# Kernel tuning notes

Measured on AMD Instinct MI355X. Metric: run time of the kernel, lower is better.

The kernel has to match this reference:

```python
import jax, jax.numpy as jnp
import numpy as np

N = 50000
E = 800000
DIM = 256
H = 8
D = DIM // H


def setup_inputs() -> dict:
    key = jax.random.key(0)
    ks = jax.random.split(key, 12)
    s = 1.0 / np.sqrt(DIM)
    return {
        "x": jax.random.normal(ks[0], (N, DIM), dtype=jnp.float32),
        "Wq": jax.random.normal(ks[1], (DIM, DIM), dtype=jnp.float32) * s,
        "bq": jax.random.normal(ks[2], (DIM,), dtype=jnp.float32) * 0.01,
        "Wk": jax.random.normal(ks[3], (DIM, DIM), dtype=jnp.float32) * s,
        "bk": jax.random.normal(ks[4], (DIM,), dtype=jnp.float32) * 0.01,
        "Wv": jax.random.normal(ks[5], (DIM, DIM), dtype=jnp.float32) * s,
        "bv": jax.random.normal(ks[6], (DIM,), dtype=jnp.float32) * 0.01,
        "Wo": jax.random.normal(ks[7], (DIM, DIM), dtype=jnp.float32) * s,
        "bo": jax.random.normal(ks[8], (DIM,), dtype=jnp.float32) * 0.01,
        "src": jax.random.randint(ks[9], (E,), 0, N, dtype=jnp.int32),
        "dst": jax.random.randint(ks[10], (E,), 0, N, dtype=jnp.int32),
    }


def reference(x, Wq, bq, Wk, bk, Wv, bv, Wo, bo, src, dst):
    # Linear projections (torch Linear: x @ W.T + b), then [N, H, D]
    q = (x @ Wq.T + bq).reshape(N, H, D)
    k = (x @ Wk.T + bk).reshape(N, H, D)
    v = (x @ Wv.T + bv).reshape(N, H, D)

    # u_dot_v: per-edge dot(queries[src], keys[dst]) -> [E, H]
    scores = jnp.einsum('ehd,ehd->eh', q[src], k[dst]) / jnp.sqrt(jnp.float32(D))

    # edge_softmax over incoming edges of each destination node
    smax = jax.ops.segment_max(scores, dst, num_segments=N)  # [N, H]
    e = jnp.exp(scores - smax[dst])                          # [E, H]
    ssum = jax.ops.segment_sum(e, dst, num_segments=N)       # [N, H]
    probs = e / ssum[dst]                                    # [E, H]

    # u_mul_e_sum: sum over incoming edges of values[src] * probs -> [N, H, D]
    out = jax.ops.segment_sum(v[src] * probs[:, :, None], dst, num_segments=N)

    out = out.reshape(N, DIM)
    return out @ Wo.T + bo  # dropout is identity at p=0 / eval
```

## Files before the change

### kernel.cpp

```cpp
#include <hip/hip_runtime.h>
#include <hip/hip_bf16.h>
#include <math.h>

#define DIMV 256
#define DV 32
#define QKVS 768

typedef __attribute__((ext_vector_type(8))) short bf16x8;
typedef __attribute__((ext_vector_type(4))) float f32x4;

#define EXPS(x) __expf(x)
#define SCORE_SCALE 0.17677669529663687f

static __device__ __forceinline__ unsigned short f2bf(float f) {
    unsigned x = __float_as_uint(f);
    x += 0x7FFF + ((x >> 16) & 1);
    return (unsigned short)(x >> 16);
}
static __device__ __forceinline__ float bf2f(unsigned short u) {
    return __uint_as_float(((unsigned)u) << 16);
}

static __device__ __forceinline__ void async16(const void* g, void* lds) {
    __builtin_amdgcn_global_load_lds(
        (const __attribute__((address_space(1))) void*)g,
        (__attribute__((address_space(3))) void*)lds, 16, 0, 0);
}


__global__ void cvt_w(const float* __restrict__ Wq, const float* __restrict__ Wk,
                      const float* __restrict__ Wv, const float* __restrict__ Wo,
                      unsigned short* __restrict__ Wcat) {
    const float* W = blockIdx.y == 0 ? Wq : blockIdx.y == 1 ? Wk : blockIdx.y == 2 ? Wv : Wo;
    int i = blockIdx.x * 256 + threadIdx.x;
    float4 v = ((const float4*)W)[i];
    ushort4 o;
    o.x = f2bf(v.x); o.y = f2bf(v.y); o.z = f2bf(v.z); o.w = f2bf(v.w);
    ((ushort4*)(Wcat + (size_t)blockIdx.y * 65536))[i] = o;
}


__global__ void zero_i32(int* __restrict__ p, int n) {
    int i = blockIdx.x * blockDim.x + threadIdx.x;
    if (i < n) p[i] = 0;
}

__global__ void count_deg(const int* __restrict__ dst, int* __restrict__ deg, int E) {
    int i = blockIdx.x * blockDim.x + threadIdx.x;
    if (i < E) atomicAdd(&deg[dst[i]], 1);
}

__global__ void block_sum(const int* __restrict__ deg, int* __restrict__ bsum, int n) {
    __shared__ int sm[256];
    int i = blockIdx.x * 256 + threadIdx.x;
    sm[threadIdx.x] = (i < n) ? deg[i] : 0;
    __syncthreads();
    for (int s = 128; s > 0; s >>= 1) {
        if (threadIdx.x < s) sm[threadIdx.x] += sm[threadIdx.x + s];
        __syncthreads();
    }
    if (threadIdx.x == 0) bsum[blockIdx.x] = sm[0];
}

__global__ void scan_bsum(int* __restrict__ bsum, int nb) {
    if (threadIdx.x == 0) {
        int r = 0;
        for (int i = 0; i < nb; ++i) { int v = bsum[i]; bsum[i] = r; r += v; }
    }
}

__global__ void scan_final(const int* __restrict__ deg, const int* __restrict__ bsum,
                           int* __restrict__ offsets, int* __restrict__ cursor, int n) {
    __shared__ int sm[256];
    int i = blockIdx.x * 256 + threadIdx.x;
    int v = (i < n) ? deg[i] : 0;
    sm[threadIdx.x] = v;
    __syncthreads();
    for (int s = 1; s < 256; s <<= 1) {
        int t = (threadIdx.x >= s) ? sm[threadIdx.x - s] : 0;
        __syncthreads();
        sm[threadIdx.x] += t;
        __syncthreads();
    }
    int excl = sm[threadIdx.x] - v + bsum[blockIdx.x];
    if (i < n) { offsets[i] = excl; cursor[i] = excl; }
    if (i == n - 1) offsets[n] = excl + v;
}

__global__ void scatter_edges(const int* __restrict__ src, const int* __restrict__ dst,
                              int* __restrict__ cursor, int* __restrict__ perm_src, int E) {
    int i = blockIdx.x * blockDim.x + threadIdx.x;
    if (i < E) {
        int pos = atomicAdd(&cursor[dst[i]], 1);
        perm_src[pos] = src[i];
    }
}


template<bool AF32, bool OF32, int OSTRIDE, int MATSTRIDE>
__global__ __launch_bounds__(256, 4)
void gemm_fused(const void* __restrict__ Ain,
                const unsigned short* __restrict__ Wcat,
                const float* __restrict__ b0, const float* __restrict__ b1,
                const float* __restrict__ b2,
                void* __restrict__ Cout, int M, int ntiles) {
    __shared__ unsigned short Bls[2][32 * 256];
    const int tid = threadIdx.x;
    const int w = tid >> 6, lane = tid & 63;
    const int rg = w >> 1, cg = w & 1;
    const int lrow = lane & 15, lkg = lane >> 4;
    const int row0 = blockIdx.x * 64;

    {
        const char* gb = (const char*)Wcat;
        #pragma unroll
        for (int i = 0; i < 4; ++i) {
            unsigned o = (unsigned)(i * 4096 + w * 1024 + lane * 16);
            unsigned srcoff = o ^ (((o >> 9) & 7u) << 4);
            async16(gb + srcoff, (char*)&Bls[0][0] + (i * 4096 + w * 1024));
        }
    }

    bf16x8 a[2][8];
    #pragma unroll
    for (int m = 0; m < 2; ++m) {
        int row = row0 + rg * 32 + m * 16 + lrow;
        row = min(row, M - 1);
        if (AF32) {
            const float* ap = (const float*)Ain + (size_t)row * DIMV + lkg * 8;
            #pragma unroll
            for (int k0 = 0; k0 < 8; ++k0) {
                float4 f0 = *(const float4*)(ap + k0 * 32);
                float4 f1 = *(const float4*)(ap + k0 * 32 + 4);
                bf16x8 r;
                r[0] = (short)f2bf(f0.x); r[1] = (short)f2bf(f0.y);
                r[2] = (short)f2bf(f0.z); r[3] = (short)f2bf(f0.w);
                r[4] = (short)f2bf(f1.x); r[5] = (short)f2bf(f1.y);
                r[6] = (short)f2bf(f1.z); r[7] = (short)f2bf(f1.w);
                a[m][k0] = r;
            }
        } else {
            const unsigned short* ap = (const unsigned short*)Ain + (size_t)row * DIMV + lkg * 8;
            #pragma unroll
            for (int k0 = 0; k0 < 8; ++k0)
                a[m][k0] = *(const bf16x8*)(ap + k0 * 32);
        }
    }
    __syncthreads();

    const int c = cg * 16 + lrow;
    for (int t = 0; t < ntiles; ++t) {
        if (t + 1 < ntiles) {
            const char* gb = (const char*)Wcat + (size_t)(t + 1) * 16384;
            #pragma unroll
            for (int i = 0; i < 4; ++i) {
                unsigned o = (unsigned)(i * 4096 + w * 1024 + lane * 16);
                unsigned srcoff = o ^ (((o >> 9) & 7u) << 4);
                async16(gb + srcoff, (char*)&Bls[(t + 1) & 1][0] + (i * 4096 + w * 1024));
            }
        }

        const char* bls = (const char*)&Bls[t & 1][0];
        f32x4 acc0 = {0.f, 0.f, 0.f, 0.f};
        f32x4 acc1 = {0.f, 0.f, 0.f, 0.f};
        #pragma unroll
        for (int k0 = 0; k0 < 8; ++k0) {
            unsigned lin = (unsigned)c * 512 + (unsigned)k0 * 64 + (unsigned)lkg * 16;
            unsigned addr = lin ^ (((unsigned)c & 7u) << 4);
            bf16x8 bf = *(const bf16x8*)(bls + addr);
            acc0 = __builtin_amdgcn_mfma_f32_16x16x32_bf16(a[0][k0], bf, acc0, 0, 0, 0);
            acc1 = __builtin_amdgcn_mfma_f32_16x16x32_bf16(a[1][k0], bf, acc1, 0, 0, 0);
        }

        int mat = t >> 3;
        const float* bp = (mat == 0) ? b0 : (mat == 1 ? b1 : b2);
        int gcol = ((t & 7) << 5) + c;
        float bias = bp[gcol];
        unsigned cbase = (unsigned)mat * MATSTRIDE + gcol;
        #pragma unroll
        for (int m = 0; m < 2; ++m) {
            f32x4 av = m ? acc1 : acc0;
            #pragma unroll
            for (int r = 0; r < 4; ++r) {
                int row = row0 + rg * 32 + m * 16 + lkg * 4 + r;
                if (row < M) {
                    float val = av[r] + bias;
                    if (OF32)
                        ((float*)Cout)[(size_t)row * OSTRIDE + cbase] = val;
                    else
                        ((unsigned short*)Cout)[(size_t)row * OSTRIDE + cbase] = f2bf(val);
                }
            }
        }
        __syncthreads();
    }
}


__global__ __launch_bounds__(256)
void node_attn(const unsigned short* __restrict__ QKV,
               const int* __restrict__ offsets, const int* __restrict__ perm_src,
               unsigned short* __restrict__ attn, int N) {
    int wid = blockIdx.x * (blockDim.x >> 6) + (threadIdx.x >> 6);
    if (wid >= N) return;
    int lane = threadIdx.x & 63;
    unsigned col = (unsigned)((lane >> 3) * DV + (lane & 7) * 4);

    ushort4 kr = *(const ushort4*)(QKV + (size_t)wid * QKVS + 256 + col);
    float k0 = bf2f(kr.x) * SCORE_SCALE, k1 = bf2f(kr.y) * SCORE_SCALE;
    float k2 = bf2f(kr.z) * SCORE_SCALE, k3 = bf2f(kr.w) * SCORE_SCALE;

    float mA = -INFINITY, lA = 0.f, aA0 = 0.f, aA1 = 0.f, aA2 = 0.f, aA3 = 0.f;
    float mB = -INFINITY, lB = 0.f, aB0 = 0.f, aB1 = 0.f, aB2 = 0.f, aB3 = 0.f;

    auto upd = [&](ushort4 qr, ushort4 vr, float& m, float& l,
                   float& a0, float& a1, float& a2, float& a3) {
        float d = bf2f(qr.x) * k0 + bf2f(qr.y) * k1 + bf2f(qr.z) * k2 + bf2f(qr.w) * k3;
        d += __shfl_xor(d, 1); d += __shfl_xor(d, 2); d += __shfl_xor(d, 4);
        float mn = fmaxf(m, d);
        float sc = EXPS(m - mn);
        float pe = EXPS(d - mn);
        l = l * sc + pe;
        a0 = a0 * sc + pe * bf2f(vr.x);
        a1 = a1 * sc + pe * bf2f(vr.y);
        a2 = a2 * sc + pe * bf2f(vr.z);
        a3 = a3 * sc + pe * bf2f(vr.w);
        m = mn;
    };

    int e0 = offsets[wid], e1 = offsets[wid + 1];
    int rem = e1 - e0;
    int S = rem >> 1;
    int p = e0;

    if (S >= 1) {
        unsigned o0 = (unsigned)perm_src[p] * QKVS + col;
        unsigned o1 = (unsigned)perm_src[p + 1] * QKVS + col;
        ushort4 qA0 = *(const ushort4*)(QKV + o0);
        ushort4 vA0 = *(const ushort4*)(QKV + o0 + 512);
        ushort4 qA1 = *(const ushort4*)(QKV + o1);
        ushort4 vA1 = *(const ushort4*)(QKV + o1 + 512);
        unsigned n0 = 0, n1 = 0;
        if (S >= 2) {
            n0 = (unsigned)perm_src[p + 2] * QKVS + col;
            n1 = (unsigned)perm_src[p + 3] * QKVS + col;
        }
        ushort4 qB0, qB1, vB0, vB1;

        int s = 0;
        while (s + 2 <= S) {
            qB0 = *(const ushort4*)(QKV + n0);
            vB0 = *(const ushort4*)(QKV + n0 + 512);
            qB1 = *(const ushort4*)(QKV + n1);
            vB1 = *(const ushort4*)(QKV + n1 + 512);
            if (s + 2 < S) {
                n0 = (unsigned)perm_src[p + 2 * s + 4] * QKVS + col;
                n1 = (unsigned)perm_src[p + 2 * s + 5] * QKVS + col;
            }
            upd(qA0, vA0, mA, lA, aA0, aA1, aA2, aA3);
            upd(qA1, vA1, mB, lB, aB0, aB1, aB2, aB3);

            if (s + 2 < S) {
                qA0 = *(const ushort4*)(QKV + n0);
                vA0 = *(const ushort4*)(QKV + n0 + 512);
                qA1 = *(const ushort4*)(QKV + n1);
                vA1 = *(const ushort4*)(QKV + n1 + 512);
                if (s + 3 < S) {
                    n0 = (unsigned)perm_src[p + 2 * s + 6] * QKVS + col;
                    n1 = (unsigned)perm_src[p + 2 * s + 7] * QKVS + col;
                }
            }
            upd(qB0, vB0, mA, lA, aA0, aA1, aA2, aA3);
            upd(qB1, vB1, mB, lB, aB0, aB1, aB2, aB3);
            s += 2;
        }
        if (s < S) {
            upd(qA0, vA0, mA, lA, aA0, aA1, aA2, aA3);
            upd(qA1, vA1, mB, lB, aB0, aB1, aB2, aB3);
        }
    }
    if (rem & 1) {
        unsigned o0 = (unsigned)perm_src[e1 - 1] * QKVS + col;
        ushort4 q0 = *(const ushort4*)(QKV + o0);
        ushort4 v0 = *(const ushort4*)(QKV + o0 + 512);
        upd(q0, v0, mA, lA, aA0, aA1, aA2, aA3);
    }

    float mn = fmaxf(mA, mB);
    float scA = (lA > 0.f) ? EXPS(mA - mn) : 0.f;
    float scB = (lB > 0.f) ? EXPS(mB - mn) : 0.f;
    float l = lA * scA + lB * scB;
    float o0 = aA0 * scA + aB0 * scB;
    float o1 = aA1 * scA + aB1 * scB;
    float o2 = aA2 * scA + aB2 * scB;
    float o3 = aA3 * scA + aB3 * scB;
    float inv = (l > 0.f) ? 1.f / l : 0.f;

    ushort4 o;
    o.x = f2bf(o0 * inv); o.y = f2bf(o1 * inv); o.z = f2bf(o2 * inv); o.w = f2bf(o3 * inv);
    *(ushort4*)(attn + (size_t)wid * DIMV + col) = o;
}


extern "C" void kernel_launch(void* const* d_in, const int* in_sizes, int n_in,
                              void* d_out, int out_size, void* d_ws, size_t ws_size,
                              hipStream_t stream) {
    const float* x  = (const float*)d_in[0];
    const float* Wq = (const float*)d_in[1];
    const float* bq = (const float*)d_in[2];
    const float* Wk = (const float*)d_in[3];
    const float* bk = (const float*)d_in[4];
    const float* Wv = (const float*)d_in[5];
    const float* bv = (const float*)d_in[6];
    const float* Wo = (const float*)d_in[7];
    const float* bo = (const float*)d_in[8];
    const int* src  = (const int*)d_in[9];
    const int* dst  = (const int*)d_in[10];
    int N = in_sizes[0] / DIMV;
    int E = in_sizes[9];
    float* out = (float*)d_out;

    char* p = (char*)d_ws;
    auto alloc = [&](size_t bytes) {
        char* r = p;
        p += (bytes + 255) & ~(size_t)255;
        return r;
    };
    unsigned short* Wcat = (unsigned short*)alloc((size_t)4 * 65536 * 2);
    unsigned short* QKV  = (unsigned short*)alloc((size_t)N * QKVS * 2);
    unsigned short* attn = (unsigned short*)alloc((size_t)N * DIMV * 2);
    int* deg             = (int*)alloc((size_t)N * 4);
    int* offsets         = (int*)alloc((size_t)(N + 1) * 4);
    int* cursor          = (int*)alloc((size_t)N * 4);
    int* perm_src        = (int*)alloc((size_t)E * 4);
    int* bsum            = (int*)alloc((size_t)1024 * 4);

    dim3 gw(64, 4);
    cvt_w<<<gw, 256, 0, stream>>>(Wq, Wk, Wv, Wo, Wcat);

    int nb = (N + 255) / 256;
    zero_i32<<<nb, 256, 0, stream>>>(deg, N);
    count_deg<<<(E + 255) / 256, 256, 0, stream>>>(dst, deg, E);
    block_sum<<<nb, 256, 0, stream>>>(deg, bsum, N);
    scan_bsum<<<1, 64, 0, stream>>>(bsum, nb);
    scan_final<<<nb, 256, 0, stream>>>(deg, bsum, offsets, cursor, N);
    scatter_edges<<<(E + 255) / 256, 256, 0, stream>>>(src, dst, cursor, perm_src, E);

    int gblocks = (N + 63) / 64;
    gemm_fused<true, false, QKVS, 256><<<gblocks, 256, 0, stream>>>(
        x, Wcat, bq, bk, bv, QKV, N, 24);

    node_attn<<<(N + 3) / 4, 256, 0, stream>>>(QKV, offsets, perm_src, attn, N);

    gemm_fused<false, true, DIMV, 0><<<gblocks, 256, 0, stream>>>(
        attn, Wcat + (size_t)3 * 65536, bo, bo, bo, out, N, 8);
}
```

Before: 326.7 us.

## Fuse degree counting and edge scatter into weight-convert and QKV GEMM kernels

Degree counting moves into the weight-conversion kernel as a grid-stride loop, and the edge scatter into CSR order moves into the QKV projection GEMM prologue. This removes two kernel launches and lets the atomic scatter overlap with the GEMM's weight prefetch. The GEMM's __syncthreads are replaced by explicit vmcnt waits plus raw s_barrier so the double-buffered async LDS loads are awaited precisely. In exchange, the atomics and scattered writes add latency before the GEMM's main loop, and the hand-counted vmcnt values are fragile.

```diff
diff --git a/kernel.cpp b/kernel.cpp
--- a/kernel.cpp
+++ b/kernel.cpp
@@ -28,26 +28,26 @@
 }
 
 
-__global__ void cvt_w(const float* __restrict__ Wq, const float* __restrict__ Wk,
-                      const float* __restrict__ Wv, const float* __restrict__ Wo,
-                      unsigned short* __restrict__ Wcat) {
+__global__ void cvt_w_count(const float* __restrict__ Wq, const float* __restrict__ Wk,
+                            const float* __restrict__ Wv, const float* __restrict__ Wo,
+                            unsigned short* __restrict__ Wcat,
+                            const int* __restrict__ dst, int* __restrict__ deg, int E) {
     const float* W = blockIdx.y == 0 ? Wq : blockIdx.y == 1 ? Wk : blockIdx.y == 2 ? Wv : Wo;
     int i = blockIdx.x * 256 + threadIdx.x;
     float4 v = ((const float4*)W)[i];
     ushort4 o;
     o.x = f2bf(v.x); o.y = f2bf(v.y); o.z = f2bf(v.z); o.w = f2bf(v.w);
     ((ushort4*)(Wcat + (size_t)blockIdx.y * 65536))[i] = o;
+
+    int gid = (blockIdx.y * gridDim.x + blockIdx.x) * 256 + threadIdx.x;
+    int nthr = gridDim.x * gridDim.y * 256;
+    for (int e = gid; e < E; e += nthr) atomicAdd(&deg[dst[e]], 1);
 }
 
 
 __global__ void zero_i32(int* __restrict__ p, int n) {
     int i = blockIdx.x * blockDim.x + threadIdx.x;
     if (i < n) p[i] = 0;
-}
-
-__global__ void count_deg(const int* __restrict__ dst, int* __restrict__ deg, int E) {
-    int i = blockIdx.x * blockDim.x + threadIdx.x;
-    if (i < E) atomicAdd(&deg[dst[i]], 1);
 }
 
 __global__ void block_sum(const int* __restrict__ deg, int* __restrict__ bsum, int n) {
@@ -87,23 +87,16 @@
     if (i == n - 1) offsets[n] = excl + v;
 }
 
-__global__ void scatter_edges(const int* __restrict__ src, const int* __restrict__ dst,
-                              int* __restrict__ cursor, int* __restrict__ perm_src, int E) {
-    int i = blockIdx.x * blockDim.x + threadIdx.x;
-    if (i < E) {
-        int pos = atomicAdd(&cursor[dst[i]], 1);
-        perm_src[pos] = src[i];
-    }
-}
-
-
-template<bool AF32, bool OF32, int OSTRIDE, int MATSTRIDE>
+
+template<bool AF32, bool OF32, int OSTRIDE, int MATSTRIDE, bool SCATTER>
 __global__ __launch_bounds__(256, 4)
 void gemm_fused(const void* __restrict__ Ain,
                 const unsigned short* __restrict__ Wcat,
                 const float* __restrict__ b0, const float* __restrict__ b1,
                 const float* __restrict__ b2,
-                void* __restrict__ Cout, int M, int ntiles) {
+                void* __restrict__ Cout, int M, int ntiles,
+                const int* __restrict__ esrc, const int* __restrict__ edst,
+                int* __restrict__ cursor, int* __restrict__ perm_src, int E) {
     __shared__ unsigned short Bls[2][32 * 256];
     const int tid = threadIdx.x;
     const int w = tid >> 6, lane = tid & 63;
@@ -118,6 +111,14 @@
             unsigned o = (unsigned)(i * 4096 + w * 1024 + lane * 16);
             unsigned srcoff = o ^ (((o >> 9) & 7u) << 4);
             async16(gb + srcoff, (char*)&Bls[0][0] + (i * 4096 + w * 1024));
+        }
+    }
+
+    if (SCATTER) {
+        int nthr = gridDim.x * 256;
+        for (int e = blockIdx.x * 256 + tid; e < E; e += nthr) {
+            int pos = atomicAdd(&cursor[edst[e]], 1);
+            perm_src[pos] = esrc[e];
         }
     }
 
@@ -146,7 +147,9 @@
                 a[m][k0] = *(const bf16x8*)(ap + k0 * 32);
         }
     }
-    __syncthreads();
+
+    asm volatile("s_waitcnt vmcnt(0)" ::: "memory");
+    __builtin_amdgcn_s_barrier();
 
     const int c = cg * 16 + lrow;
     for (int t = 0; t < ntiles; ++t) {
@@ -158,7 +161,11 @@
                 unsigned srcoff = o ^ (((o >> 9) & 7u) << 4);
                 async16(gb + srcoff, (char*)&Bls[(t + 1) & 1][0] + (i * 4096 + w * 1024));
             }
-        }
+            asm volatile("s_waitcnt vmcnt(4)" ::: "memory");
+        } else {
+            asm volatile("s_waitcnt vmcnt(0)" ::: "memory");
+        }
+        __builtin_amdgcn_s_barrier();
 
         const char* bls = (const char*)&Bls[t & 1][0];
         f32x4 acc0 = {0.f, 0.f, 0.f, 0.f};
@@ -192,7 +199,7 @@
                 }
             }
         }
-        __syncthreads();
+        __builtin_amdgcn_s_barrier();
     }
 }
 
@@ -335,23 +342,22 @@
     int* perm_src        = (int*)alloc((size_t)E * 4);
     int* bsum            = (int*)alloc((size_t)1024 * 4);
 
-    dim3 gw(64, 4);
-    cvt_w<<<gw, 256, 0, stream>>>(Wq, Wk, Wv, Wo, Wcat);
-
     int nb = (N + 255) / 256;
     zero_i32<<<nb, 256, 0, stream>>>(deg, N);
-    count_deg<<<(E + 255) / 256, 256, 0, stream>>>(dst, deg, E);
+    dim3 gw(64, 4);
+    cvt_w_count<<<gw, 256, 0, stream>>>(Wq, Wk, Wv, Wo, Wcat, dst, deg, E);
+
     block_sum<<<nb, 256, 0, stream>>>(deg, bsum, N);
     scan_bsum<<<1, 64, 0, stream>>>(bsum, nb);
     scan_final<<<nb, 256, 0, stream>>>(deg, bsum, offsets, cursor, N);
-    scatter_edges<<<(E + 255) / 256, 256, 0, stream>>>(src, dst, cursor, perm_src, E);
 
     int gblocks = (N + 63) / 64;
-    gemm_fused<true, false, QKVS, 256><<<gblocks, 256, 0, stream>>>(
-        x, Wcat, bq, bk, bv, QKV, N, 24);
+    gemm_fused<true, false, QKVS, 256, true><<<gblocks, 256, 0, stream>>>(
+        x, Wcat, bq, bk, bv, QKV, N, 24, src, dst, cursor, perm_src, E);
 
     node_attn<<<(N + 3) / 4, 256, 0, stream>>>(QKV, offsets, perm_src, attn, N);
 
-    gemm_fused<false, true, DIMV, 0><<<gblocks, 256, 0, stream>>>(
-        attn, Wcat + (size_t)3 * 65536, bo, bo, bo, out, N, 8);
-}
+    gemm_fused<false, true, DIMV, 0, false><<<gblocks, 256, 0, stream>>>(
+        attn, Wcat + (size_t)3 * 65536, bo, bo, bo, out, N, 8,
+        nullptr, nullptr, nullptr, nullptr, 0);
+}
```

New measurement: 336.7 us. +3.1%, slower.
